# Kernel tuning notes

Measured on AMD Instinct MI355X. Metric: run time of the kernel, lower is better.

Reference implementation:

```python
import jax, jax.numpy as jnp
import numpy as np

E = 2048      # embed_size
H = 16        # heads_size
D_HEAD = E // H          # 128
D_ROPE = 32
SPLIT = D_HEAD - D_ROPE  # 96
C = 512       # d_kv_comp
B, S = 2, 2048
ROT_SCALE = 40.0


def _rotary_emb(seq_len):
    # inv_freq has d_rope//4 entries; emb is [S, d_rope//2]
    half = D_ROPE // 2
    inv_freq = 1.0 / (10000.0 ** (jnp.arange(0, half, 2, dtype=jnp.float32) / half))
    t = jnp.arange(seq_len, dtype=jnp.float32) / ROT_SCALE
    freqs = jnp.einsum('i,j->ij', t, inv_freq)
    return jnp.concatenate([freqs, freqs], axis=-1)  # [S, d_rope//2]


def _rotate_half(x):
    x1, x2 = jnp.split(x, 2, axis=-1)
    return jnp.concatenate([-x2, x1], axis=-1)


def _apply_rotary(x, cos, sin):
    rd = cos.shape[-1]
    x_rot, x_base = x[..., :rd], x[..., rd:]
    x_rot = x_rot * cos + _rotate_half(x_rot) * sin
    return jnp.concatenate([x_rot, x_base], axis=-1)


def setup_inputs() -> dict:
    key = jax.random.key(0)
    ks = jax.random.split(key, 10)

    def xav(k, shape):
        fan_in, fan_out = shape
        lim = float(np.sqrt(6.0 / (fan_in + fan_out)))
        return jax.random.uniform(k, shape, jnp.float32, -lim, lim)

    return {
        'h': jax.random.normal(ks[0], (B, S, E), jnp.float32),
        'W_dkv': xav(ks[1], (E, C)), 'b_dkv': jnp.zeros((C,), jnp.float32),
        'W_dq':  xav(ks[2], (E, C)), 'b_dq':  jnp.zeros((C,), jnp.float32),
        'W_uk':  xav(ks[3], (C, H * SPLIT)),  'b_uk': jnp.zeros((H * SPLIT,), jnp.float32),
        'W_uv':  xav(ks[4], (C, H * D_HEAD)), 'b_uv': jnp.zeros((H * D_HEAD,), jnp.float32),
        'W_uq':  xav(ks[5], (C, H * SPLIT)),  'b_uq': jnp.zeros((H * SPLIT,), jnp.float32),
        'W_qr':  xav(ks[6], (C, H * D_ROPE)), 'b_qr': jnp.zeros((H * D_ROPE,), jnp.float32),
        'W_kr':  xav(ks[7], (E, H * D_ROPE)), 'b_kr': jnp.zeros((H * D_ROPE,), jnp.float32),
        'W_out': xav(ks[8], (H * D_HEAD, E)), 'b_out': jnp.zeros((E,), jnp.float32),
    }


def reference(h, W_dkv, b_dkv, W_dq, b_dq, W_uk, b_uk, W_uv, b_uv,
              W_uq, b_uq, W_qr, b_qr, W_kr, b_kr, W_out, b_out):
    Bq, Sq, _ = h.shape
    c_kv = h @ W_dkv + b_dkv                                   # [B,S,C]
    k = (c_kv @ W_uk + b_uk).reshape(Bq, Sq, H, SPLIT)
    v = (c_kv @ W_uv + b_uv).reshape(Bq, Sq, H, D_HEAD)
    c_q = h @ W_dq + b_dq
    q_base = (c_q @ W_uq + b_uq).reshape(Bq, Sq, H, SPLIT)
    q_rot = (c_q @ W_qr + b_qr).reshape(Bq, Sq, H, D_ROPE)

    emb = _rotary_emb(Sq)                                      # [S, d_rope//2]
    cos = jnp.cos(emb)[None, :, None, :]
    sin = jnp.sin(emb)[None, :, None, :]
    q_rot = _apply_rotary(q_rot, cos, sin)
    k_rot = _apply_rotary((h @ W_kr + b_kr).reshape(Bq, Sq, H, D_ROPE), cos, sin)

    q = jnp.concatenate([q_base, q_rot], axis=-1)              # [B,S,H,d_head]
    k_full = jnp.concatenate([k, k_rot], axis=-1)

    scores = jnp.einsum('bqhd,bkhd->bhqk', q, k_full) / jnp.sqrt(jnp.float32(D_HEAD))
    causal = jnp.tril(jnp.ones((Sq, Sq), dtype=bool))
    scores = jnp.where(causal[None, None], scores, -jnp.inf)
    attn = jax.nn.softmax(scores, axis=-1)
    out = jnp.einsum('bhqk,bkhd->bqhd', attn, v).reshape(Bq, Sq, H * D_HEAD)
    out = out @ W_out + b_out
    return out, c_kv, k_rot
```

## Files before the change

kernel.cpp:

```cpp
#include <hip/hip_runtime.h>
#include <hip/hip_bf16.h>

#define B_   2
#define S_   2048
#define E_   2048
#define H_   16
#define DH_  128
#define DR_  32
#define SP_  96
#define C_   512
#define M_   (B_ * S_)

#define LOG2E 1.4426950408889634f

typedef __attribute__((ext_vector_type(8))) short short8;
typedef __attribute__((ext_vector_type(4))) float floatx4;

__device__ __forceinline__ float bfu(unsigned short u) {
  return __uint_as_float((unsigned)u << 16);
}
__device__ __forceinline__ unsigned short f2bf(float f) {
  unsigned u = __float_as_uint(f);
  return (unsigned short)((u + 0x7fff + ((u >> 16) & 1)) >> 16);
}

__device__ __forceinline__ void gload16(const void* g, void* l) {
  __builtin_amdgcn_global_load_lds(
      (const __attribute__((address_space(1))) void*)g,
      (__attribute__((address_space(3))) void*)l, 16, 0, 0);
}

struct TEnt { const float* W; unsigned short* Wt; int K, N, ntiles, nx; };
struct TTab { TEnt e[8]; };

__global__ __launch_bounds__(256) void prep_kernel(
    const float* __restrict__ hsrc, unsigned short* __restrict__ hdst,
    TTab tab) {
  if (blockIdx.x < 8192) {
    size_t i = ((size_t)blockIdx.x * 256 + threadIdx.x) * 4;
    float4 v = *(const float4*)(hsrc + i);
    ushort4 w;
    w.x = f2bf(v.x); w.y = f2bf(v.y); w.z = f2bf(v.z); w.w = f2bf(v.w);
    *(ushort4*)(hdst + i) = w;
    return;
  }
  __shared__ unsigned short T[32][33];
  int rem = blockIdx.x - 8192;
  const float* W = nullptr; unsigned short* Wt = nullptr;
  int K = 0, N = 0, nx = 1;
  bool done = false;
#pragma unroll
  for (int j = 0; j < 8; j++) {
    if (!done) {
      if (rem < tab.e[j].ntiles) {
        W = tab.e[j].W; Wt = tab.e[j].Wt;
        K = tab.e[j].K; N = tab.e[j].N; nx = tab.e[j].nx;
        done = true;
      } else {
        rem -= tab.e[j].ntiles;
      }
    }
  }
  int n0 = (rem % nx) * 32, k0 = (rem / nx) * 32;
  int t = threadIdx.x, lane = t & 31, grp = t >> 5;
#pragma unroll
  for (int p = 0; p < 4; p++) {
    int k = p * 8 + grp;
    T[lane][k] = f2bf(W[(size_t)(k0 + k) * N + n0 + lane]);
  }
  __syncthreads();
#pragma unroll
  for (int p = 0; p < 4; p++) {
    int n = p * 8 + grp;
    Wt[(size_t)(n0 + n) * K + k0 + lane] = T[n][lane];
  }
}

struct Seg {
  float* outF;
  unsigned short* outB;
  const float* bias;
  const float* biasM;
  float* krotF;
  int orow, chunk, gstride, obase, nstart, ileave, rope;
  float oscale;
};

template <bool BK64>
__device__ __forceinline__ void gemm_body(
    const unsigned short* __restrict__ A, const unsigned short* __restrict__ W,
    int K, int bm, int bn, const Seg& sg) {
  __shared__ unsigned short As0[BK64 ? 128 * 64 : 128 * 32];
  __shared__ unsigned short Bs0[BK64 ? 128 * 64 : 128 * 32];
  __shared__ unsigned short As1[BK64 ? 128 * 64 : 128 * 32];
  __shared__ unsigned short Bs1[BK64 ? 128 * 64 : 128 * 32];
  int tid = threadIdx.x;
  int lane = tid & 63, wave = tid >> 6;
  int l16 = lane & 15, quad = lane >> 4;
  int wm = (wave & 1) * 64, wn = (wave >> 1) * 64;

  floatx4 acc[4][4];
#pragma unroll
  for (int mt = 0; mt < 4; mt++)
#pragma unroll
    for (int nt = 0; nt < 4; nt++) acc[mt][nt] = (floatx4){0.f, 0.f, 0.f, 0.f};

  int c0 = wave * 2, c1 = c0 + 1;
  int srow = lane >> 2, scol = (lane & 3) * 8;
  const unsigned short* Ag0 = A + (size_t)(bm + c0 * 16 + srow) * K + scol;
  const unsigned short* Ag1 = A + (size_t)(bm + c1 * 16 + srow) * K + scol;
  const unsigned short* Bg0 = W + (size_t)(bn + c0 * 16 + srow) * K + scol;
  const unsigned short* Bg1 = W + (size_t)(bn + c1 * 16 + srow) * K + scol;

#define GSTAGE(kk, Asb, Bsb) do {            \
    gload16(Ag0 + (kk), &Asb[c0 * 512]);     \
    gload16(Ag1 + (kk), &Asb[c1 * 512]);     \
    gload16(Bg0 + (kk), &Bsb[c0 * 512]);     \
    gload16(Bg1 + (kk), &Bsb[c1 * 512]); } while (0)

#define GSTAGE64(kk, Asb, Bsb) do {                 \
    gload16(Ag0 + (kk),      &Asb[c0 * 512]);       \
    gload16(Ag1 + (kk),      &Asb[c1 * 512]);       \
    gload16(Bg0 + (kk),      &Bsb[c0 * 512]);       \
    gload16(Bg1 + (kk),      &Bsb[c1 * 512]);       \
    gload16(Ag0 + (kk) + 32, &Asb[4096 + c0 * 512]);\
    gload16(Ag1 + (kk) + 32, &Asb[4096 + c1 * 512]);\
    gload16(Bg0 + (kk) + 32, &Bsb[4096 + c0 * 512]);\
    gload16(Bg1 + (kk) + 32, &Bsb[4096 + c1 * 512]); } while (0)

#define GCOMPUTE(Ap, Bp) do {                                              \
    const unsigned short* Asb = (Ap);                                      \
    const unsigned short* Bsb = (Bp);                                      \
    short8 af[4], bfv[4];                                                  \
    _Pragma("unroll")                                                      \
    for (int mt = 0; mt < 4; mt++)                                         \
      af[mt] = *(const short8*)&Asb[(wm + mt * 16 + l16) * 32 + quad * 8]; \
    _Pragma("unroll")                                                      \
    for (int nt = 0; nt < 4; nt++)                                         \
      bfv[nt] = *(const short8*)&Bsb[(wn + nt * 16 + l16) * 32 + quad * 8];\
    _Pragma("unroll")                                                      \
    for (int mt = 0; mt < 4; mt++)                                         \
      _Pragma("unroll")                                                    \
      for (int nt = 0; nt < 4; nt++)                                       \
        acc[mt][nt] = __builtin_amdgcn_mfma_f32_16x16x32_bf16(             \
            af[mt], bfv[nt], acc[mt][nt], 0, 0, 0); } while (0)

  if constexpr (BK64) {
    GSTAGE64(0, As0, Bs0);
    __syncthreads();
    for (int k0 = 0; k0 < K; k0 += 128) {
      GSTAGE64(k0 + 64, As1, Bs1);
      GCOMPUTE(&As0[0], &Bs0[0]);
      GCOMPUTE(&As0[4096], &Bs0[4096]);
      __syncthreads();
      if (k0 + 128 < K) GSTAGE64(k0 + 128, As0, Bs0);
      GCOMPUTE(&As1[0], &Bs1[0]);
      GCOMPUTE(&As1[4096], &Bs1[4096]);
      __syncthreads();
    }
  } else {
    GSTAGE(0, As0, Bs0);
    __syncthreads();
    for (int k0 = 0; k0 < K; k0 += 64) {
      GSTAGE(k0 + 32, As1, Bs1);
      GCOMPUTE(&As0[0], &Bs0[0]);
      __syncthreads();
      if (k0 + 64 < K) GSTAGE(k0 + 64, As0, Bs0);
      GCOMPUTE(&As1[0], &Bs1[0]);
      __syncthreads();
    }
  }
#undef GSTAGE
#undef GSTAGE64
#undef GCOMPUTE

#pragma unroll
  for (int mt = 0; mt < 4; mt++) {
    int m0 = bm + wm + mt * 16 + quad * 4;
    float bm4[4] = {0.f, 0.f, 0.f, 0.f};
    if (sg.biasM) {
#pragma unroll
      for (int r = 0; r < 4; r++) bm4[r] = sg.biasM[m0 + r];
    }
#pragma unroll
    for (int nt = 0; nt < 4; nt++) {
      int n = bn + wn + nt * 16 + l16;
      int nl = n - sg.nstart;
      float bv = sg.biasM ? 0.f : sg.bias[nl];
      int ncol = sg.obase + (nl / sg.chunk) * sg.gstride + (nl % sg.chunk);
      if (sg.ileave)
        ncol = (ncol & ~31) | ((ncol & 15) << 1) | ((ncol >> 4) & 1);
      bool rot_half = sg.rope && ((nl & 31) < 16);
#pragma unroll
      for (int r = 0; r < 4; r++) {
        float val = (acc[mt][nt][r] + (sg.biasM ? bm4[r] : bv)) * sg.oscale;
        if (rot_half) {
          int j = l16 & 7;
          int srw = (m0 + r) & (S_ - 1);
          float ang = ((float)srw / 40.0f) *
                      exp2f(-1.6609640474436813f * (float)j);
          float cc = __cosf(ang), ss = __sinf(ang);
          float part = __shfl_xor(val, 8);
          val = (l16 < 8) ? (val * cc - part * ss) : (val * cc + part * ss);
        }
        if (sg.rope == 1 && sg.krotF)
          sg.krotF[(size_t)(m0 + r) * (H_ * DR_) + nl] = val;
        size_t idx = (size_t)(m0 + r) * sg.orow + ncol;
        if (sg.outF) sg.outF[idx] = val;
        if (sg.outB) sg.outB[idx] = f2bf(val);
      }
    }
  }
}

template <bool BK64>
__global__ __launch_bounds__(256) void mfma_gemm(
    const unsigned short* __restrict__ A, const unsigned short* __restrict__ Wt,
    Seg s0, Seg s1, Seg s2, int K) {
  int gx = gridDim.x;
  int nwg = gx * gridDim.y;
  int flat = blockIdx.y * gx + blockIdx.x;
  int w = (flat & 7) * (nwg >> 3) + (flat >> 3);
  int by = w / gx, bx = w - by * gx;
  int bm = by * 128, bn = bx * 128;
  Seg sg = (bn >= s2.nstart) ? s2 : ((bn >= s1.nstart) ? s1 : s0);
  gemm_body<BK64>(A, Wt, K, bm, bn, sg);
}

__global__ __launch_bounds__(256) void fused_gemm3(
    const unsigned short* __restrict__ ckv, const unsigned short* __restrict__ cq,
    const unsigned short* __restrict__ wuk, const unsigned short* __restrict__ wuv,
    const unsigned short* __restrict__ wuq,
    unsigned short* __restrict__ kbf, unsigned short* __restrict__ vtbf,
    unsigned short* __restrict__ qbf,
    const float* __restrict__ b_uk, const float* __restrict__ b_uv,
    const float* __restrict__ b_uq, const float* __restrict__ b_qr,
    float qscale) {
  int flat = blockIdx.x;
  int w = (flat & 7) * 176 + (flat >> 3);
  const unsigned short* A; const unsigned short* W;
  int bm, bn;
  Seg sg;
  sg.outF = nullptr; sg.oscale = 1.f; sg.ileave = 0; sg.nstart = 0;
  sg.rope = 0; sg.krotF = nullptr;
  if (w < 384) {
    int by = w / 12, bx = w - by * 12;
    bm = by * 128; bn = bx * 128;
    A = ckv; W = wuk;
    sg.outB = kbf; sg.bias = b_uk; sg.biasM = nullptr;
    sg.orow = 2048; sg.chunk = SP_; sg.gstride = DH_; sg.obase = 0;
  } else if (w < 896) {
    int w2 = w - 384;
    int by = w2 >> 5, bx = w2 & 31;
    bm = by * 128; bn = bx * 128;
    A = wuv; W = ckv;
    sg.outB = vtbf; sg.bias = nullptr; sg.biasM = b_uv;
    sg.orow = M_; sg.chunk = M_; sg.gstride = M_; sg.obase = 0; sg.ileave = 1;
  } else {
    int w3 = w - 896;
    int by = w3 >> 4, bx = w3 & 15;
    bm = by * 128; bn = bx * 128;
    A = cq; W = wuq;
    sg.outB = qbf; sg.biasM = nullptr; sg.orow = 2048; sg.oscale = qscale;
    if (bn >= 1536) {
      sg.bias = b_qr; sg.chunk = DR_; sg.gstride = DH_; sg.obase = SP_;
      sg.nstart = 1536; sg.rope = 2;
    } else {
      sg.bias = b_uq; sg.chunk = SP_; sg.gstride = DH_; sg.obase = 0;
    }
  }
  gemm_body<false>(A, W, 512, bm, bn, sg);
}

#define PST 72
__global__ __launch_bounds__(256, 2) void attn_kernel(
    const unsigned short* __restrict__ qf, const unsigned short* __restrict__ kf,
    const unsigned short* __restrict__ vt, unsigned short* __restrict__ ao) {
  __shared__ unsigned short Ks[2][64 * 128];
  __shared__ unsigned short Vs[2][128 * 64];
  __shared__ unsigned short Ps[4][16 * PST];

  int bid0 = blockIdx.x;
  int xcd  = bid0 & 7;
  int idx  = bid0 >> 3;
  int r_   = idx >> 5;
  int q_   = idx & 31;
  int bh   = xcd * 4 + (q_ >> 3);
  int jp   = r_ ? (15 - (q_ & 7)) : (q_ & 7);
  int h    = bh & 15;
  int b    = bh >> 4;
  int jjh  = 31 - jp;
  int jjl  = jp;
  int q0h  = jjh << 6, q0l = jjl << 6;
  int nchunks = jjh + 1;

  int tid  = threadIdx.x;
  int wave = tid >> 6;
  int lane = tid & 63;
  int l16  = lane & 15;
  int quad = lane >> 4;
  int x7   = l16 & 7;

  int krow = tid >> 2;
  int kst  = (tid & 3) * 4;
  int vrow = tid >> 1;
  int vst  = (tid & 1) * 4;
  const unsigned short* kg =
      kf + ((size_t)(b * S_ + krow)) * 2048 + h * 128 + kst * 8;
  const unsigned short* vg =
      vt + ((size_t)(h * 128 + vrow)) * 4096 + b * 2048 + vst * 8;
  int kwl[4], vwl[4];
#pragma unroll
  for (int i = 0; i < 4; i++) {
    kwl[i] = krow * 128 + (((kst + i) ^ (krow & 7)) * 8);
    vwl[i] = vrow * 64  + (((vst + i) ^ (vrow & 7)) * 8);
  }

  short8 qfh[4], qfl[4];
  {
    const unsigned short* qb =
        qf + ((size_t)(b * S_ + q0h + wave * 16 + l16)) * 2048 + h * 128 + quad * 8;
#pragma unroll
    for (int c = 0; c < 4; c++) qfh[c] = *(const short8*)(qb + c * 32);
  }
  {
    const unsigned short* qb =
        qf + ((size_t)(b * S_ + q0l + wave * 16 + l16)) * 2048 + h * 128 + quad * 8;
#pragma unroll
    for (int c = 0; c < 4; c++) qfl[c] = *(const short8*)(qb + c * 32);
  }

  floatx4 OaccH[8], OaccL[8];
#pragma unroll
  for (int dt = 0; dt < 8; dt++) {
    OaccH[dt] = (floatx4){0.f, 0.f, 0.f, 0.f};
    OaccL[dt] = (floatx4){0.f, 0.f, 0.f, 0.f};
  }
  float lpH[4] = {0.f, 0.f, 0.f, 0.f};
  float lpL[4] = {0.f, 0.f, 0.f, 0.f};
  int qgh = q0h + wave * 16;
  int qgl = q0l + wave * 16;

#define SCOMPUTE(QF, OC, LP, QG, DIAG) do {                                   \
    const unsigned short* Kc = Ks[cur];                                       \
    const unsigned short* Vc = Vs[cur];                                       \
    floatx4 sv[4];                                                            \
    _Pragma("unroll")                                                         \
    for (int nt = 0; nt < 4; nt++) sv[nt] = (floatx4){0.f, 0.f, 0.f, 0.f};    \
    __builtin_amdgcn_s_setprio(1);                                            \
    _Pragma("unroll")                                                         \
    for (int nt = 0; nt < 4; nt++)                                            \
      _Pragma("unroll")                                                       \
      for (int c = 0; c < 4; c++) {                                           \
        short8 kfr = *(const short8*)&Kc[(nt * 16 + l16) * 128 +              \
                                         ((4 * c + quad) ^ x7) * 8];          \
        sv[nt] = __builtin_amdgcn_mfma_f32_16x16x32_bf16(QF[c], kfr, sv[nt],  \
                                                         0, 0, 0);            \
      }                                                                       \
    __builtin_amdgcn_s_setprio(0);                                            \
    unsigned short* P = Ps[wave];                                             \
    _Pragma("unroll")                                                         \
    for (int ks = 0; ks < 2; ks++)                                            \
      _Pragma("unroll")                                                       \
      for (int r = 0; r < 4; r++) {                                           \
        float p0 = exp2f(fminf(sv[2 * ks][r], 80.f));                         \
        float p1 = exp2f(fminf(sv[2 * ks + 1][r], 80.f));                     \
        if (DIAG) {                                                           \
          int q_r = QG + quad * 4 + r;                                        \
          int kc0 = kt0 + ks * 32 + l16;                                      \
          if (kc0 > q_r)      p0 = 0.f;                                       \
          if (kc0 + 16 > q_r) p1 = 0.f;                                       \
        }                                                                     \
        unsigned pk;                                                          \
        asm("v_cvt_pk_bf16_f32 %0, %1, %2" : "=v"(pk) : "v"(p0), "v"(p1));    \
        *(unsigned*)&P[(quad * 4 + r) * PST + ks * 32 + 2 * l16] = pk;        \
        LP[r] += p0 + p1;                                                     \
      }                                                                       \
    short8 pf0 = *(const short8*)&P[l16 * PST + quad * 8];                    \
    short8 pf1 = *(const short8*)&P[l16 * PST + 32 + quad * 8];               \
    __builtin_amdgcn_s_setprio(1);                                            \
    _Pragma("unroll")                                                         \
    for (int dt = 0; dt < 8; dt++) {                                          \
      short8 vf0 = *(const short8*)&Vc[(dt * 16 + l16) * 64 +                 \
                                       ((quad) ^ x7) * 8];                    \
      OC[dt] = __builtin_amdgcn_mfma_f32_16x16x32_bf16(pf0, vf0, OC[dt],      \
                                                       0, 0, 0);              \
      short8 vf1 = *(const short8*)&Vc[(dt * 16 + l16) * 64 +                 \
                                       ((4 + quad) ^ x7) * 8];                \
      OC[dt] = __builtin_amdgcn_mfma_f32_16x16x32_bf16(pf1, vf1, OC[dt],      \
                                                       0, 0, 0);              \
    }                                                                         \
    __builtin_amdgcn_s_setprio(0);                                            \
  } while (0)

  short8 kr[4], vr[4];
#pragma unroll
  for (int i = 0; i < 4; i++) {
    kr[i] = *(const short8*)(kg + i * 8);
    vr[i] = *(const short8*)(vg + i * 8);
  }
#pragma unroll
  for (int i = 0; i < 4; i++) {
    *(short8*)&Ks[0][kwl[i]] = kr[i];
    *(short8*)&Vs[0][vwl[i]] = vr[i];
  }
#pragma unroll
  for (int i = 0; i < 4; i++) {
    kr[i] = *(const short8*)(kg + 131072 + i * 8);
    vr[i] = *(const short8*)(vg + 64 + i * 8);
  }
  __syncthreads();

  int cur = 0;
  for (int t = 0; t < nchunks; t++) {
#pragma unroll
    for (int i = 0; i < 4; i++) {
      *(short8*)&Ks[cur ^ 1][kwl[i]] = kr[i];
      *(short8*)&Vs[cur ^ 1][vwl[i]] = vr[i];
    }
    {
      int tf = (t + 2 < nchunks) ? t + 2 : nchunks - 1;
      const unsigned short* ksrc = kg + (size_t)tf * 131072;
      const unsigned short* vsrc = vg + tf * 64;
#pragma unroll
      for (int i = 0; i < 4; i++) {
        kr[i] = *(const short8*)(ksrc + i * 8);
        vr[i] = *(const short8*)(vsrc + i * 8);
      }
    }
    int kt0 = t << 6;
    SCOMPUTE(qfh, OaccH, lpH, qgh, (t == jjh));
    if (t <= jjl) SCOMPUTE(qfl, OaccL, lpL, qgl, (t == jjl));
    __syncthreads();
    cur ^= 1;
  }
#undef SCOMPUTE

#pragma unroll
  for (int side = 0; side < 2; side++) {
    floatx4* OC = side ? OaccL : OaccH;
    float*   LP = side ? lpL : lpH;
    int qg = (side ? qgl : qgh) + quad * 4;
    float linv[4];
#pragma unroll
    for (int r = 0; r < 4; r++) {
      float ls = LP[r];
#pragma unroll
      for (int sh = 1; sh < 16; sh <<= 1) ls += __shfl_xor(ls, sh);
      linv[r] = 1.0f / ls;
    }
#pragma unroll
    for (int r = 0; r < 4; r++) {
      unsigned short* dst =
          ao + ((size_t)(b * S_ + qg + r)) * 2048 + h * 128 + l16;
#pragma unroll
      for (int dt = 0; dt < 8; dt++) dst[dt * 16] = f2bf(OC[dt][r] * linv[r]);
    }
  }
}

static inline Seg mkseg(float* oF, unsigned short* oB, const float* bias,
                        const float* biasM, int orow, int chunk, int gstride,
                        int obase, int nstart, int ileave, float oscale,
                        int rope, float* krotF) {
  Seg s;
  s.outF = oF; s.outB = oB; s.bias = bias; s.biasM = biasM; s.krotF = krotF;
  s.orow = orow; s.chunk = chunk; s.gstride = gstride;
  s.obase = obase; s.nstart = nstart; s.ileave = ileave; s.rope = rope;
  s.oscale = oscale;
  return s;
}
static inline Seg segnone() {
  return mkseg(nullptr, nullptr, nullptr, nullptr, 1, 1, 1, 0, 0x7fffffff,
               0, 1.f, 0, nullptr);
}
static inline TEnt mktent(const float* W, unsigned short* Wt, int K, int N,
                          int ntiles, int nx) {
  TEnt e;
  e.W = W; e.Wt = Wt; e.K = K; e.N = N; e.ntiles = ntiles; e.nx = nx;
  return e;
}

extern "C" void kernel_launch(void* const* d_in, const int* in_sizes, int n_in,
                              void* d_out, int out_size, void* d_ws, size_t ws_size,
                              hipStream_t stream) {
  const float* h     = (const float*)d_in[0];
  const float* W_dkv = (const float*)d_in[1];
  const float* b_dkv = (const float*)d_in[2];
  const float* W_dq  = (const float*)d_in[3];
  const float* b_dq  = (const float*)d_in[4];
  const float* W_uk  = (const float*)d_in[5];
  const float* b_uk  = (const float*)d_in[6];
  const float* W_uv  = (const float*)d_in[7];
  const float* b_uv  = (const float*)d_in[8];
  const float* W_uq  = (const float*)d_in[9];
  const float* b_uq  = (const float*)d_in[10];
  const float* W_qr  = (const float*)d_in[11];
  const float* b_qr  = (const float*)d_in[12];
  const float* W_kr  = (const float*)d_in[13];
  const float* b_kr  = (const float*)d_in[14];
  const float* W_out = (const float*)d_in[15];
  const float* b_out = (const float*)d_in[16];

  float* out      = (float*)d_out;
  float* out_ckv  = out + (size_t)M_ * E_;
  float* out_krot = out_ckv + (size_t)M_ * C_;

  unsigned short* w16 = (unsigned short*)d_ws;
  unsigned short* h_bf   = w16;
  unsigned short* q_bf   = w16 + 8388608;
  unsigned short* k_bf   = w16 + 16777216;
  unsigned short* vt_bf  = w16 + 25165824;
  unsigned short* ao_bf  = w16 + 33554432;
  unsigned short* ckv_bf = w16 + 41943040;
  unsigned short* cq_bf  = w16 + 44040192;
  unsigned short* Wt_dkv = w16 + 46137344;
  unsigned short* Wt_dq  = w16 + 47185920;
  unsigned short* Wt_kr  = w16 + 48234496;
  unsigned short* Wt_uk  = w16 + 49283072;
  unsigned short* Wt_uv  = w16 + 50069504;
  unsigned short* Wt_uq  = w16 + 51118080;
  unsigned short* Wt_qr  = w16 + 51904512;
  unsigned short* Wt_out = w16 + 52166656;
  (void)Wt_qr;

  dim3 blk256(256);
  const float qscale = 0.08838834764831845f * LOG2E;

  TTab tab;
  tab.e[0] = mktent(W_dkv, Wt_dkv, E_, C_,       1024, 16);
  tab.e[1] = mktent(W_dq,  Wt_dq,  E_, C_,       1024, 16);
  tab.e[2] = mktent(W_kr,  Wt_kr,  E_, H_ * DR_, 1024, 16);
  tab.e[3] = mktent(W_uk,  Wt_uk,  C_, H_ * SP_,  768, 48);
  tab.e[4] = mktent(W_uv,  Wt_uv,  C_, H_ * DH_, 1024, 64);
  tab.e[5] = mktent(W_uq,  Wt_uq,  C_, H_ * SP_,  768, 48);
  tab.e[6] = mktent(W_qr,  w16 + 51904512, C_, H_ * DR_,  256, 16);
  tab.e[7] = mktent(W_out, Wt_out, E_, E_,       4096, 64);
  prep_kernel<<<18176, blk256, 0, stream>>>(h, h_bf, tab);

  mfma_gemm<true><<<dim3(1536 / 128, M_ / 128), blk256, 0, stream>>>(
      h_bf, Wt_dkv,
      mkseg(out_ckv, ckv_bf, b_dkv, nullptr, C_, C_, C_, 0, 0, 0, 1.f, 0, nullptr),
      mkseg(nullptr, cq_bf,  b_dq,  nullptr, C_, C_, C_, 0, 512, 0, 1.f, 0, nullptr),
      mkseg(nullptr, k_bf,   b_kr,  nullptr, 2048, DR_, DH_, SP_, 1024, 0, 1.f,
            1, out_krot),
      E_);

  fused_gemm3<<<1408, blk256, 0, stream>>>(
      ckv_bf, cq_bf, Wt_uk, Wt_uv, Wt_uq, k_bf, vt_bf, q_bf,
      b_uk, b_uv, b_uq, b_qr, qscale);

  attn_kernel<<<B_ * H_ * 16, blk256, 0, stream>>>(q_bf, k_bf, vt_bf, ao_bf);

  mfma_gemm<true><<<dim3(E_ / 128, M_ / 128), blk256, 0, stream>>>(
      ao_bf, Wt_out,
      mkseg(out, nullptr, b_out, nullptr, E_, E_, E_, 0, 0, 0, 1.f, 0, nullptr),
      segnone(), segnone(), E_);
}
```

Measured before the change: 343.3 us.

## Use direct global-to-LDS loads and fuse high/low query tiles in attention

Replaces the register-staged K/V prefetch, which did global loads into registers and then LDS stores, with direct global-to-LDS loads (gload16) issued one chunk ahead with a pre-swizzled source layout. The high and low query tiles now share each K/V fragment read inside one fused body, which removes duplicate LDS reads and interleaves their MFMAs. The P staging buffer is also split per side and given an XOR-swizzled layout instead of padding. The prefetch distance drops from two chunks to one, and the gload16 helper is assumed to be defined in the hidden code, so that part carries some latency and correctness risk.

```diff
diff --git a/kernel.cpp b/kernel.cpp
--- a/kernel.cpp
+++ b/kernel.cpp
@@ -272,13 +272,13 @@
   gemm_body<false>(A, W, 512, bm, bn, sg);
 }
 
-#define PST 72
 __global__ __launch_bounds__(256, 2) void attn_kernel(
     const unsigned short* __restrict__ qf, const unsigned short* __restrict__ kf,
     const unsigned short* __restrict__ vt, unsigned short* __restrict__ ao) {
   __shared__ unsigned short Ks[2][64 * 128];
   __shared__ unsigned short Vs[2][128 * 64];
-  __shared__ unsigned short Ps[4][16 * PST];
+  __shared__ unsigned short PsH[4][16 * 64];
+  __shared__ unsigned short PsL[4][16 * 64];
 
   int bid0 = blockIdx.x;
   int xcd  = bid0 & 7;
@@ -301,20 +301,30 @@
   int quad = lane >> 4;
   int x7   = l16 & 7;
 
-  int krow = tid >> 2;
-  int kst  = (tid & 3) * 4;
-  int vrow = tid >> 1;
-  int vst  = (tid & 1) * 4;
-  const unsigned short* kg =
-      kf + ((size_t)(b * S_ + krow)) * 2048 + h * 128 + kst * 8;
-  const unsigned short* vg =
-      vt + ((size_t)(h * 128 + vrow)) * 4096 + b * 2048 + vst * 8;
-  int kwl[4], vwl[4];
-#pragma unroll
-  for (int i = 0; i < 4; i++) {
-    kwl[i] = krow * 128 + (((kst + i) ^ (krow & 7)) * 8);
-    vwl[i] = vrow * 64  + (((vst + i) ^ (vrow & 7)) * 8);
-  }
+  const unsigned short *kp0, *kp1, *kp2, *kp3, *vp0, *vp1, *vp2, *vp3;
+  {
+    int l4 = lane >> 4, l3 = lane >> 3;
+#define KSRC(i) (kf + ((size_t)(b * S_ + 16 * wave + 4 * (i) + l4)) * 2048 + \
+                 h * 128 + (((lane & 15) ^ ((16 * wave + 4 * (i) + l4) & 7)) * 8))
+#define VSRC(i) (vt + ((size_t)(h * 128 + 32 * wave + 8 * (i) + l3)) * 4096 + \
+                 b * 2048 + (((lane & 7) ^ ((32 * wave + 8 * (i) + l3) & 7)) * 8))
+    kp0 = KSRC(0); kp1 = KSRC(1); kp2 = KSRC(2); kp3 = KSRC(3);
+    vp0 = VSRC(0); vp1 = VSRC(1); vp2 = VSRC(2); vp3 = VSRC(3);
+#undef KSRC
+#undef VSRC
+  }
+  int ldso = wave * 2048;
+
+#define STAGE(tt, bb) do {                                                   \
+    size_t ko_ = (size_t)(tt) * 131072; int vo_ = (tt) * 64;                 \
+    gload16(kp0 + ko_, &Ks[bb][ldso]);                                       \
+    gload16(kp1 + ko_, &Ks[bb][ldso + 512]);                                 \
+    gload16(kp2 + ko_, &Ks[bb][ldso + 1024]);                                \
+    gload16(kp3 + ko_, &Ks[bb][ldso + 1536]);                                \
+    gload16(vp0 + vo_, &Vs[bb][ldso]);                                       \
+    gload16(vp1 + vo_, &Vs[bb][ldso + 512]);                                 \
+    gload16(vp2 + vo_, &Vs[bb][ldso + 1024]);                                \
+    gload16(vp3 + vo_, &Vs[bb][ldso + 1536]); } while (0)
 
   short8 qfh[4], qfl[4];
   {
@@ -341,30 +351,13 @@
   int qgh = q0h + wave * 16;
   int qgl = q0l + wave * 16;
 
-#define SCOMPUTE(QF, OC, LP, QG, DIAG) do {                                   \
-    const unsigned short* Kc = Ks[cur];                                       \
-    const unsigned short* Vc = Vs[cur];                                       \
-    floatx4 sv[4];                                                            \
-    _Pragma("unroll")                                                         \
-    for (int nt = 0; nt < 4; nt++) sv[nt] = (floatx4){0.f, 0.f, 0.f, 0.f};    \
-    __builtin_amdgcn_s_setprio(1);                                            \
-    _Pragma("unroll")                                                         \
-    for (int nt = 0; nt < 4; nt++)                                            \
-      _Pragma("unroll")                                                       \
-      for (int c = 0; c < 4; c++) {                                           \
-        short8 kfr = *(const short8*)&Kc[(nt * 16 + l16) * 128 +              \
-                                         ((4 * c + quad) ^ x7) * 8];          \
-        sv[nt] = __builtin_amdgcn_mfma_f32_16x16x32_bf16(QF[c], kfr, sv[nt],  \
-                                                         0, 0, 0);            \
-      }                                                                       \
-    __builtin_amdgcn_s_setprio(0);                                            \
-    unsigned short* P = Ps[wave];                                             \
+#define SMAX(SV, PW, LP, QG, DIAG) do {                                       \
     _Pragma("unroll")                                                         \
     for (int ks = 0; ks < 2; ks++)                                            \
       _Pragma("unroll")                                                       \
       for (int r = 0; r < 4; r++) {                                           \
-        float p0 = exp2f(fminf(sv[2 * ks][r], 80.f));                         \
-        float p1 = exp2f(fminf(sv[2 * ks + 1][r], 80.f));                     \
+        float p0 = exp2f(fminf(SV[2 * ks][r], 80.f));                         \
+        float p1 = exp2f(fminf(SV[2 * ks + 1][r], 80.f));                     \
         if (DIAG) {                                                           \
           int q_r = QG + quad * 4 + r;                                        \
           int kc0 = kt0 + ks * 32 + l16;                                      \
@@ -373,68 +366,82 @@
         }                                                                     \
         unsigned pk;                                                          \
         asm("v_cvt_pk_bf16_f32 %0, %1, %2" : "=v"(pk) : "v"(p0), "v"(p1));    \
-        *(unsigned*)&P[(quad * 4 + r) * PST + ks * 32 + 2 * l16] = pk;        \
+        int prow = quad * 4 + r;                                              \
+        int pslot = (ks * 4 + (l16 >> 2)) ^ (prow & 7);                       \
+        *(unsigned*)&PW[prow * 64 + pslot * 8 + (l16 & 3) * 2] = pk;          \
         LP[r] += p0 + p1;                                                     \
+      } } while (0)
+
+#define FBODY(LOACT) do {                                                     \
+    const unsigned short* Kc = Ks[cur];                                       \
+    const unsigned short* Vc = Vs[cur];                                       \
+    floatx4 svH[4], svL[4];                                                   \
+    _Pragma("unroll")                                                         \
+    for (int nt = 0; nt < 4; nt++) {                                          \
+      svH[nt] = (floatx4){0.f, 0.f, 0.f, 0.f};                                \
+      svL[nt] = (floatx4){0.f, 0.f, 0.f, 0.f};                                \
+    }                                                                         \
+    __builtin_amdgcn_s_setprio(1);                                            \
+    _Pragma("unroll")                                                         \
+    for (int nt = 0; nt < 4; nt++)                                            \
+      _Pragma("unroll")                                                       \
+      for (int c = 0; c < 4; c++) {                                           \
+        short8 kfr = *(const short8*)&Kc[(nt * 16 + l16) * 128 +              \
+                                         ((4 * c + quad) ^ x7) * 8];          \
+        svH[nt] = __builtin_amdgcn_mfma_f32_16x16x32_bf16(qfh[c], kfr,        \
+                                                          svH[nt], 0, 0, 0);  \
+        if (LOACT)                                                            \
+          svL[nt] = __builtin_amdgcn_mfma_f32_16x16x32_bf16(qfl[c], kfr,      \
+                                                            svL[nt], 0, 0, 0);\
       }                                                                       \
-    short8 pf0 = *(const short8*)&P[l16 * PST + quad * 8];                    \
-    short8 pf1 = *(const short8*)&P[l16 * PST + 32 + quad * 8];               \
+    __builtin_amdgcn_s_setprio(0);                                            \
+    unsigned short* PwH = PsH[wave];                                          \
+    unsigned short* PwL = PsL[wave];                                          \
+    SMAX(svH, PwH, lpH, qgh, (t == jjh));                                     \
+    if (LOACT) SMAX(svL, PwL, lpL, qgl, (t == jjl));                          \
+    short8 pfH0 = *(const short8*)&PwH[l16 * 64 + (quad ^ x7) * 8];           \
+    short8 pfH1 = *(const short8*)&PwH[l16 * 64 + (((4 + quad)) ^ x7) * 8];   \
+    short8 pfL0, pfL1;                                                        \
+    if (LOACT) {                                                              \
+      pfL0 = *(const short8*)&PwL[l16 * 64 + (quad ^ x7) * 8];                \
+      pfL1 = *(const short8*)&PwL[l16 * 64 + (((4 + quad)) ^ x7) * 8];        \
+    }                                                                         \
     __builtin_amdgcn_s_setprio(1);                                            \
     _Pragma("unroll")                                                         \
     for (int dt = 0; dt < 8; dt++) {                                          \
       short8 vf0 = *(const short8*)&Vc[(dt * 16 + l16) * 64 +                 \
-                                       ((quad) ^ x7) * 8];                    \
-      OC[dt] = __builtin_amdgcn_mfma_f32_16x16x32_bf16(pf0, vf0, OC[dt],      \
-                                                       0, 0, 0);              \
+                                       (quad ^ x7) * 8];                      \
+      OaccH[dt] = __builtin_amdgcn_mfma_f32_16x16x32_bf16(pfH0, vf0,          \
+                                                          OaccH[dt], 0, 0, 0);\
+      if (LOACT)                                                              \
+        OaccL[dt] = __builtin_amdgcn_mfma_f32_16x16x32_bf16(pfL0, vf0,        \
+                                                            OaccL[dt], 0,0,0);\
       short8 vf1 = *(const short8*)&Vc[(dt * 16 + l16) * 64 +                 \
                                        ((4 + quad) ^ x7) * 8];                \
-      OC[dt] = __builtin_amdgcn_mfma_f32_16x16x32_bf16(pf1, vf1, OC[dt],      \
-                                                       0, 0, 0);              \
+      OaccH[dt] = __builtin_amdgcn_mfma_f32_16x16x32_bf16(pfH1, vf1,          \
+                                                          OaccH[dt], 0, 0, 0);\
+      if (LOACT)                                                              \
+        OaccL[dt] = __builtin_amdgcn_mfma_f32_16x16x32_bf16(pfL1, vf1,        \
+                                                            OaccL[dt], 0,0,0);\
     }                                                                         \
     __builtin_amdgcn_s_setprio(0);                                            \
   } while (0)
 
-  short8 kr[4], vr[4];
-#pragma unroll
-  for (int i = 0; i < 4; i++) {
-    kr[i] = *(const short8*)(kg + i * 8);
-    vr[i] = *(const short8*)(vg + i * 8);
-  }
-#pragma unroll
-  for (int i = 0; i < 4; i++) {
-    *(short8*)&Ks[0][kwl[i]] = kr[i];
-    *(short8*)&Vs[0][vwl[i]] = vr[i];
-  }
-#pragma unroll
-  for (int i = 0; i < 4; i++) {
-    kr[i] = *(const short8*)(kg + 131072 + i * 8);
-    vr[i] = *(const short8*)(vg + 64 + i * 8);
-  }
+  STAGE(0, 0);
   __syncthreads();
 
   int cur = 0;
   for (int t = 0; t < nchunks; t++) {
-#pragma unroll
-    for (int i = 0; i < 4; i++) {
-      *(short8*)&Ks[cur ^ 1][kwl[i]] = kr[i];
-      *(short8*)&Vs[cur ^ 1][vwl[i]] = vr[i];
-    }
-    {
-      int tf = (t + 2 < nchunks) ? t + 2 : nchunks - 1;
-      const unsigned short* ksrc = kg + (size_t)tf * 131072;
-      const unsigned short* vsrc = vg + tf * 64;
-#pragma unroll
-      for (int i = 0; i < 4; i++) {
-        kr[i] = *(const short8*)(ksrc + i * 8);
-        vr[i] = *(const short8*)(vsrc + i * 8);
-      }
-    }
+    if (t + 1 < nchunks) STAGE(t + 1, cur ^ 1);
     int kt0 = t << 6;
-    SCOMPUTE(qfh, OaccH, lpH, qgh, (t == jjh));
-    if (t <= jjl) SCOMPUTE(qfl, OaccL, lpL, qgl, (t == jjl));
+    if (t <= jjl) FBODY(true);
+    else          FBODY(false);
     __syncthreads();
     cur ^= 1;
   }
-#undef SCOMPUTE
+#undef FBODY
+#undef SMAX
+#undef STAGE
 
 #pragma unroll
   for (int side = 0; side < 2; side++) {
```

After: 345.1 us. Within noise of the previous version (+0.5%).
